# Optimization experiments

Measured on AMD Instinct MI355X. Metric: run time of the kernel, lower is better.

Reference implementation:

```python
import jax, jax.numpy as jnp
import numpy as np

N_NODES = 100000
N_EDGES = 3200000
IN_FEATS = 256
N_UNITS = 32
OUT_FEATS = 40


def setup_inputs() -> dict:
    key = jax.random.key(0)
    k = jax.random.split(key, 6)
    return {
        "x": jax.random.normal(k[0], (N_NODES, IN_FEATS), dtype=jnp.float32),
        "W1": jax.random.normal(k[1], (IN_FEATS, N_UNITS), dtype=jnp.float32) / np.sqrt(IN_FEATS),
        "b1": jnp.zeros((N_UNITS,), dtype=jnp.float32),
        "W2": jax.random.normal(k[2], (N_UNITS, OUT_FEATS), dtype=jnp.float32) / np.sqrt(N_UNITS),
        "b2": jnp.zeros((OUT_FEATS,), dtype=jnp.float32),
        "src": jax.random.randint(k[3], (N_EDGES,), 0, N_NODES, dtype=jnp.int32),
        "dst": jax.random.randint(k[4], (N_EDGES,), 0, N_NODES, dtype=jnp.int32),
    }


def _graph_conv(x, W, b, src, dst, inv_sqrt_out, inv_sqrt_in, n_nodes):
    # DGL GraphConv, norm='both':
    #   out = D_in^{-1/2} * A^T * (D_out^{-1/2} * x @ W) + b
    # Apply the dense transform first (in_feats >= out_feats here) so edge
    # messages are gathered at the narrow width.
    h = (x * inv_sqrt_out[:, None]) @ W              # [N, F_out]
    msgs = h[src]                                     # [E, F_out] gather
    agg = jax.ops.segment_sum(msgs, dst, num_segments=n_nodes)  # [N, F_out]
    return agg * inv_sqrt_in[:, None] + b


def reference(x, W1, b1, W2, b2, src, dst):
    n = x.shape[0]
    ones = jnp.ones((src.shape[0],), dtype=x.dtype)
    out_deg = jax.ops.segment_sum(ones, src, num_segments=n)
    in_deg = jax.ops.segment_sum(ones, dst, num_segments=n)
    inv_sqrt_out = jax.lax.rsqrt(jnp.maximum(out_deg, 1.0))  # DGL clamps deg>=1
    inv_sqrt_in = jax.lax.rsqrt(jnp.maximum(in_deg, 1.0))

    h = _graph_conv(x, W1, b1, src, dst, inv_sqrt_out, inv_sqrt_in, n)
    h = jax.nn.relu(h)
    # dropout(p=0.5, training=False) is identity in eval mode
    h = _graph_conv(h, W2, b2, src, dst, inv_sqrt_out, inv_sqrt_in, n)
    return jax.nn.log_softmax(h, axis=1)
```

## Files before the change

### kernel.cpp

```cpp
#include <hip/hip_runtime.h>
#include <hip/hip_bf16.h>
#include <math.h>

#define N_NODES 100000
#define N_EDGES 3200000
#define IN_FEATS 256
#define N_UNITS 32
#define OUT_FEATS 40

#define NPB 64
#define BSHIFT 6
#define NB 1563
#define CAP 4096

#define NC 49
#define CSHIFT 11
#define CHUNK 8192
#define NBLK ((N_EDGES + CHUNK - 1) / CHUNK)
#define WIN 128

#define ODS2 65536
#define OD_WORDS 16384
#define OD_NSL 2
#define OD_S 192

__global__ void __launch_bounds__(256) outdeg_hist_kernel(const int* __restrict__ src,
                                                          unsigned* __restrict__ partials) {
    __shared__ unsigned lh[OD_WORDS];
    int slice = blockIdx.x / OD_S;
    int stripe = blockIdx.x % OD_S;
    for (int i = threadIdx.x; i < OD_WORDS; i += 256) lh[i] = 0;
    __syncthreads();
    int lo = slice * ODS2;
    const int4* s4 = (const int4*)src;
    const int total4 = N_EDGES / 4;
    for (int i = stripe * 256 + threadIdx.x; i < total4; i += OD_S * 256) {
        int4 v = s4[i];
        unsigned a = (unsigned)(v.x - lo); if (a < ODS2) atomicAdd(&lh[a >> 2], 1u << ((a & 3) * 8));
        unsigned b = (unsigned)(v.y - lo); if (b < ODS2) atomicAdd(&lh[b >> 2], 1u << ((b & 3) * 8));
        unsigned c = (unsigned)(v.z - lo); if (c < ODS2) atomicAdd(&lh[c >> 2], 1u << ((c & 3) * 8));
        unsigned d = (unsigned)(v.w - lo); if (d < ODS2) atomicAdd(&lh[d >> 2], 1u << ((d & 3) * 8));
    }
    __syncthreads();
    unsigned* dstp = partials + (size_t)blockIdx.x * OD_WORDS;
    for (int i = threadIdx.x; i < OD_WORDS; i += 256) dstp[i] = lh[i];
}

__global__ void __launch_bounds__(256) outdeg_reduce_kernel(const unsigned* __restrict__ partials,
                                                            float* __restrict__ inv_out) {
    int i = blockIdx.x * 256 + threadIdx.x;
    if (i >= N_NODES / 4) return;
    int slice = i >> 14;
    int w = i & (OD_WORDS - 1);
    const unsigned* p = partials + (size_t)slice * OD_S * OD_WORDS + w;
    unsigned s = 0;
    #pragma unroll 8
    for (int j = 0; j < OD_S; ++j) s += p[(size_t)j * OD_WORDS];
    float4 r;
    r.x = rsqrtf(fmaxf((float)(s & 0xFF), 1.0f));
    r.y = rsqrtf(fmaxf((float)((s >> 8) & 0xFF), 1.0f));
    r.z = rsqrtf(fmaxf((float)((s >> 16) & 0xFF), 1.0f));
    r.w = rsqrtf(fmaxf((float)(s >> 24), 1.0f));
    *(float4*)(inv_out + 4 * i) = r;
}

__global__ void __launch_bounds__(256) count_kernel(const int* __restrict__ dst,
                                                    int* __restrict__ bucket_count) {
    __shared__ int lh[NB];
    for (int i = threadIdx.x; i < NB; i += 256) lh[i] = 0;
    __syncthreads();
    const int4* d4 = (const int4*)dst;
    const int total4 = N_EDGES / 4;
    for (int i = blockIdx.x * 256 + threadIdx.x; i < total4; i += gridDim.x * 256) {
        int4 v = d4[i];
        atomicAdd(&lh[v.x >> BSHIFT], 1);
        atomicAdd(&lh[v.y >> BSHIFT], 1);
        atomicAdd(&lh[v.z >> BSHIFT], 1);
        atomicAdd(&lh[v.w >> BSHIFT], 1);
    }
    __syncthreads();
    for (int i = threadIdx.x; i < NB; i += 256)
        if (lh[i]) atomicAdd(&bucket_count[i], lh[i]);
}

__global__ void __launch_bounds__(1024) scan_kernel(const int* __restrict__ bucket_count,
                                                    int* __restrict__ gbase,
                                                    int* __restrict__ gcursor,
                                                    int* __restrict__ gbaseA,
                                                    int* __restrict__ gcursorA) {
    __shared__ int ps[1024];
    int t = threadIdx.x;
    int i0 = 2 * t, i1 = 2 * t + 1;
    int a = (i0 < NB) ? bucket_count[i0] : 0;
    int b = (i1 < NB) ? bucket_count[i1] : 0;
    ps[t] = a + b;
    __syncthreads();
    for (int off = 1; off < 1024; off <<= 1) {
        int v = (t >= off) ? ps[t - off] : 0;
        __syncthreads();
        ps[t] += v;
        __syncthreads();
    }
    int excl = ps[t] - (a + b);
    if (i0 < NB) { gbase[i0] = excl; gcursor[i0] = excl; }
    if (i1 <= NB) { gbase[i1] = excl + a; if (i1 < NB) gcursor[i1] = excl + a; }
    __syncthreads();
    if (t < NC) { int v = gbase[t * 32]; gbaseA[t] = v; gcursorA[t] = v; }
    if (t == NC) gbaseA[NC] = N_EDGES;
}

__global__ void __launch_bounds__(512) binA_kernel(const int* __restrict__ src,
                                                   const int* __restrict__ dst,
                                                   int* __restrict__ gcursorA,
                                                   unsigned* __restrict__ pairsA) {
    __shared__ unsigned sortedA[CHUNK];
    __shared__ int hist[NC];
    __shared__ int lstart[NC];
    __shared__ int cur[NC];
    __shared__ int gres[NC];
    int tid = threadIdx.x;
    int e0 = blockIdx.x * CHUNK;
    int cnt = min(CHUNK, N_EDGES - e0);
    unsigned es[16], ed[16];
    #pragma unroll
    for (int r = 0; r < 16; ++r) {
        int idx = tid + 512 * r;
        if (idx < cnt) { es[r] = src[e0 + idx]; ed[r] = dst[e0 + idx]; }
    }
    if (tid < NC) hist[tid] = 0;
    __syncthreads();
    #pragma unroll
    for (int r = 0; r < 16; ++r) {
        int idx = tid + 512 * r;
        if (idx < cnt) atomicAdd(&hist[ed[r] >> CSHIFT], 1);
    }
    __syncthreads();
    if (tid < 64) {
        int v = (tid < NC) ? hist[tid] : 0;
        int inc = v;
        #pragma unroll
        for (int off = 1; off < 64; off <<= 1) {
            int u = __shfl_up(inc, off, 64);
            if ((tid & 63) >= off) inc += u;
        }
        if (tid < NC) {
            int ls = inc - v;
            lstart[tid] = ls;
            cur[tid] = ls;
            gres[tid] = atomicAdd(&gcursorA[tid], v) - ls;
        }
    }
    __syncthreads();
    #pragma unroll
    for (int r = 0; r < 16; ++r) {
        int idx = tid + 512 * r;
        if (idx < cnt) {
            int c = ed[r] >> CSHIFT;
            int pos = atomicAdd(&cur[c], 1);
            sortedA[pos] = es[r] | ((ed[r] & ((1u << CSHIFT) - 1)) << 17);
        }
    }
    __syncthreads();
    for (int i = tid; i < cnt; i += 512) {
        int lo = 0, hi = NC - 1;
        while (lo < hi) { int mid = (lo + hi + 1) >> 1; if (lstart[mid] <= i) lo = mid; else hi = mid - 1; }
        pairsA[gres[lo] + i] = sortedA[i];
    }
}

__global__ void __launch_bounds__(512) binB_kernel(const unsigned* __restrict__ pairsA,
                                                   const int* __restrict__ gbaseA,
                                                   int* __restrict__ gcursor,
                                                   unsigned* __restrict__ pairs) {
    __shared__ unsigned sortedB[CHUNK];
    __shared__ int hist[WIN];
    __shared__ int lstart[WIN];
    __shared__ int cur[WIN];
    __shared__ int gres[WIN];
    __shared__ int gA[NC + 1];
    int tid = threadIdx.x;
    if (tid <= NC) gA[tid] = gbaseA[tid];
    if (tid < WIN) hist[tid] = 0;
    int e0 = blockIdx.x * CHUNK;
    int cnt = min(CHUNK, N_EDGES - e0);
    __syncthreads();
    int c0 = 0;
    { int lo = 0, hi = NC - 1;
      while (lo < hi) { int mid = (lo + hi + 1) >> 1; if (gA[mid] <= e0) lo = mid; else hi = mid - 1; }
      c0 = lo; }
    int w0 = c0 * 32;
    unsigned pv[16]; short fw[16];
    int c = c0;
    #pragma unroll
    for (int r = 0; r < 16; ++r) {
        int idx = tid + 512 * r;
        if (idx < cnt) {
            int pos = e0 + idx;
            while (pos >= gA[c + 1]) ++c;
            unsigned p = pairsA[pos];
            unsigned srcid = p & 0x1FFFF;
            unsigned dl11 = (p >> 17) & 0x7FF;
            int wi = (c - c0) * 32 + (int)(dl11 >> 6);
            atomicAdd(&hist[wi], 1);
            pv[r] = srcid | ((dl11 & 63u) << 24);
            fw[r] = (short)wi;
        }
    }
    __syncthreads();
    if (tid < 64) {
        int v0 = hist[2 * tid], v1 = hist[2 * tid + 1];
        int s = v0 + v1;
        int inc = s;
        #pragma unroll
        for (int off = 1; off < 64; off <<= 1) {
            int u = __shfl_up(inc, off, 64);
            if ((tid & 63) >= off) inc += u;
        }
        int excl = inc - s;
        lstart[2 * tid] = excl;      cur[2 * tid] = excl;
        lstart[2 * tid + 1] = excl + v0; cur[2 * tid + 1] = excl + v0;
        int f0 = w0 + 2 * tid, f1 = f0 + 1;
        gres[2 * tid]     = (f0 < NB) ? (atomicAdd(&gcursor[f0], v0) - excl) : 0;
        gres[2 * tid + 1] = (f1 < NB) ? (atomicAdd(&gcursor[f1], v1) - (excl + v0)) : 0;
    }
    __syncthreads();
    #pragma unroll
    for (int r = 0; r < 16; ++r) {
        int idx = tid + 512 * r;
        if (idx < cnt) {
            int pos = atomicAdd(&cur[fw[r]], 1);
            sortedB[pos] = pv[r];
        }
    }
    __syncthreads();
    for (int i = tid; i < cnt; i += 512) {
        int lo = 0, hi = WIN - 1;
        while (lo < hi) { int mid = (lo + hi + 1) >> 1; if (lstart[mid] <= i) lo = mid; else hi = mid - 1; }
        pairs[gres[lo] + i] = sortedB[i];
    }
}

__global__ void __launch_bounds__(256) gemm1_kernel(
        const float* __restrict__ x, const float* __restrict__ W1,
        const float* __restrict__ inv_out, float* __restrict__ h, int N) {
    __shared__ float Ws[IN_FEATS * N_UNITS];
    for (int idx = threadIdx.x; idx < IN_FEATS * N_UNITS; idx += 256)
        Ws[idx] = W1[idx];
    __syncthreads();
    unsigned t = blockIdx.x * 256 + threadIdx.x;
    unsigned n = t >> 2;
    if (n >= (unsigned)N) return;
    unsigned j0 = (t & 3) * 8;
    float acc[8] = {0, 0, 0, 0, 0, 0, 0, 0};
    const float4* xr = (const float4*)(x + (size_t)n * IN_FEATS);
    #pragma unroll 4
    for (int k4 = 0; k4 < IN_FEATS / 4; ++k4) {
        float4 xv = xr[k4];
        const float* wk = Ws + (k4 * 4) * N_UNITS + j0;
        #pragma unroll
        for (int jj = 0; jj < 8; ++jj) acc[jj] = fmaf(xv.x, wk[jj], acc[jj]);
        #pragma unroll
        for (int jj = 0; jj < 8; ++jj) acc[jj] = fmaf(xv.y, wk[N_UNITS + jj], acc[jj]);
        #pragma unroll
        for (int jj = 0; jj < 8; ++jj) acc[jj] = fmaf(xv.z, wk[2 * N_UNITS + jj], acc[jj]);
        #pragma unroll
        for (int jj = 0; jj < 8; ++jj) acc[jj] = fmaf(xv.w, wk[3 * N_UNITS + jj], acc[jj]);
    }
    float io = inv_out[n];
    float* hr = h + (size_t)n * N_UNITS + j0;
    #pragma unroll
    for (int jj = 0; jj < 8; ++jj) hr[jj] = acc[jj] * io;
}

template <bool LAYER1>
__global__ void __launch_bounds__(256) gather_kernel(
        const float* __restrict__ in, const unsigned* __restrict__ pairs,
        const int* __restrict__ gbase, const float* __restrict__ inv_out,
        const float* __restrict__ b1, float* __restrict__ outbuf,
        float* __restrict__ inv_in) {
    __shared__ int sorted[CAP];
    __shared__ int cnt[NPB];
    __shared__ int start[NPB + 1];
    __shared__ int cur[NPB];
    __shared__ float b1s[N_UNITS];
    int tid = threadIdx.x;
    int b = blockIdx.x;
    int ebeg = gbase[b];
    int ecnt = min(gbase[b + 1] - ebeg, CAP);
    if (tid < NPB) cnt[tid] = 0;
    if (LAYER1 && tid < N_UNITS) b1s[tid] = b1[tid];
    __syncthreads();

    unsigned stash[16];
    #pragma unroll
    for (int r = 0; r < 16; ++r) {
        int idx = tid + 256 * r;
        if (idx < ecnt) {
            unsigned p = pairs[ebeg + idx];
            stash[r] = p;
            atomicAdd(&cnt[p >> 24], 1);
        }
    }
    __syncthreads();

    if (tid < 64) {
        int v = cnt[tid];
        int inc = v;
        #pragma unroll
        for (int off = 1; off < 64; off <<= 1) {
            int u = __shfl_up(inc, off, 64);
            if (tid >= off) inc += u;
        }
        start[tid + 1] = inc;
        cur[tid] = inc - v;
        if (tid == 0) start[0] = 0;
    }
    __syncthreads();

    #pragma unroll
    for (int r = 0; r < 16; ++r) {
        int idx = tid + 256 * r;
        if (idx < ecnt) {
            unsigned p = stash[r];
            int pos = atomicAdd(&cur[p >> 24], 1);
            sorted[pos] = (int)(p & 0xFFFFFF);
        }
    }
    __syncthreads();

    int w = tid >> 6;
    int lane = tid & 63;
    int q = lane & 7;
    int eo = lane >> 3;
    int nd0 = b * NPB;
    #pragma unroll 1
    for (int p = 0; p < 16; ++p) {
        int nd = w * 16 + p;
        int n = nd0 + nd;
        int beg = start[nd];
        int end = start[nd + 1];
        float ax0 = 0.f, ay0 = 0.f, az0 = 0.f, aw0 = 0.f;
        float ax1 = 0.f, ay1 = 0.f, az1 = 0.f, aw1 = 0.f;
        int e = beg + eo;
        for (; e + 8 < end; e += 16) {
            int s0 = sorted[e];
            int s1 = sorted[e + 8];
            float4 v0 = *(const float4*)(in + (size_t)s0 * N_UNITS + q * 4);
            float4 v1 = *(const float4*)(in + (size_t)s1 * N_UNITS + q * 4);
            ax0 += v0.x; ay0 += v0.y; az0 += v0.z; aw0 += v0.w;
            ax1 += v1.x; ay1 += v1.y; az1 += v1.z; aw1 += v1.w;
        }
        if (e < end) {
            float4 v = *(const float4*)(in + (size_t)sorted[e] * N_UNITS + q * 4);
            ax0 += v.x; ay0 += v.y; az0 += v.z; aw0 += v.w;
        }
        e += 8;
        if (e < end) {
            float4 v = *(const float4*)(in + (size_t)sorted[e] * N_UNITS + q * 4);
            ax1 += v.x; ay1 += v.y; az1 += v.z; aw1 += v.w;
        }
        float sx = ax0 + ax1, sy = ay0 + ay1, sz = az0 + az1, sw = aw0 + aw1;
        #pragma unroll
        for (int st = 8; st < 64; st <<= 1) {
            sx += __shfl_xor(sx, st, 64);
            sy += __shfl_xor(sy, st, 64);
            sz += __shfl_xor(sz, st, 64);
            sw += __shfl_xor(sw, st, 64);
        }
        if (eo == 0 && n < N_NODES) {
            if (LAYER1) {
                float ii = rsqrtf(fmaxf((float)(end - beg), 1.0f));
                float io = inv_out[n];
                float4 r;
                r.x = fmaxf(fmaf(sx, ii, b1s[q * 4 + 0]), 0.0f) * io;
                r.y = fmaxf(fmaf(sy, ii, b1s[q * 4 + 1]), 0.0f) * io;
                r.z = fmaxf(fmaf(sz, ii, b1s[q * 4 + 2]), 0.0f) * io;
                r.w = fmaxf(fmaf(sw, ii, b1s[q * 4 + 3]), 0.0f) * io;
                *(float4*)(outbuf + (size_t)n * N_UNITS + q * 4) = r;
                if (q == 0) inv_in[n] = ii;
            } else {
                *(float4*)(outbuf + (size_t)n * N_UNITS + q * 4) =
                    make_float4(sx, sy, sz, sw);
            }
        }
    }
}

__global__ void __launch_bounds__(256) finalize_kernel(
        const float* __restrict__ agg2, const float* __restrict__ inv_in,
        const float* __restrict__ W2, const float* __restrict__ b2,
        float* __restrict__ out, int N) {
    __shared__ float W2s[N_UNITS * OUT_FEATS];
    __shared__ float b2s[OUT_FEATS];
    for (int i = threadIdx.x; i < N_UNITS * OUT_FEATS; i += 256) W2s[i] = W2[i];
    if (threadIdx.x < OUT_FEATS) b2s[threadIdx.x] = b2[threadIdx.x];
    __syncthreads();
    int n = blockIdx.x * 256 + threadIdx.x;
    if (n >= N) return;
    float a[N_UNITS];
    const float4* ar = (const float4*)(agg2 + (size_t)n * N_UNITS);
    #pragma unroll
    for (int qq = 0; qq < N_UNITS / 4; ++qq) {
        float4 v = ar[qq];
        a[qq * 4 + 0] = v.x; a[qq * 4 + 1] = v.y; a[qq * 4 + 2] = v.z; a[qq * 4 + 3] = v.w;
    }
    float ii = inv_in[n];
    float s[OUT_FEATS];
    #pragma unroll
    for (int o = 0; o < OUT_FEATS; ++o) s[o] = 0.0f;
    #pragma unroll
    for (int k = 0; k < N_UNITS; ++k) {
        float ak = a[k];
        #pragma unroll
        for (int o = 0; o < OUT_FEATS; ++o) s[o] = fmaf(ak, W2s[k * OUT_FEATS + o], s[o]);
    }
    float mx = -INFINITY;
    #pragma unroll
    for (int o = 0; o < OUT_FEATS; ++o) {
        s[o] = fmaf(s[o], ii, b2s[o]);
        mx = fmaxf(mx, s[o]);
    }
    float sum = 0.0f;
    #pragma unroll
    for (int o = 0; o < OUT_FEATS; ++o) sum += __expf(s[o] - mx);
    float lse = mx + __logf(sum);
    #pragma unroll
    for (int o = 0; o < OUT_FEATS; ++o) s[o] -= lse;
    float4* orow4 = (float4*)(out + (size_t)n * OUT_FEATS);
    #pragma unroll
    for (int qq = 0; qq < OUT_FEATS / 4; ++qq)
        orow4[qq] = make_float4(s[qq * 4], s[qq * 4 + 1], s[qq * 4 + 2], s[qq * 4 + 3]);
}

extern "C" void kernel_launch(void* const* d_in, const int* in_sizes, int n_in,
                              void* d_out, int out_size, void* d_ws, size_t ws_size,
                              hipStream_t stream) {
    const float* x   = (const float*)d_in[0];
    const float* W1  = (const float*)d_in[1];
    const float* b1  = (const float*)d_in[2];
    const float* W2  = (const float*)d_in[3];
    const float* b2  = (const float*)d_in[4];
    const int*   src = (const int*)d_in[5];
    const int*   dst = (const int*)d_in[6];
    float* out = (float*)d_out;

    char* base = (char*)d_ws;
    float*    inv_out      = (float*)(base);
    int*      bucket_count = (int*)(base + 400000L);
    int*      gbaseA       = (int*)(base + 406400L);
    int*      gcursorA     = (int*)(base + 406912L);
    int*      gbase        = (int*)(base + 408192L);
    int*      gcursor      = (int*)(base + 416384L);
    float*    inv_in       = (float*)(base + 424576L);
    unsigned* pairs        = (unsigned*)(base + 824576L);
    float*    h            = (float*)(base + 13624576L);
    float*    rprime       = (float*)(base + 26424576L);
    float*    agg2         = (float*)(base + 39224576L);
    unsigned* pairsA       = (unsigned*)h;
    unsigned* partials     = (unsigned*)rprime;

    hipMemsetAsync(bucket_count, 0, 8192L, stream);

    outdeg_hist_kernel<<<OD_NSL * OD_S, 256, 0, stream>>>(src, partials);
    outdeg_reduce_kernel<<<(N_NODES / 4 + 255) / 256, 256, 0, stream>>>(partials, inv_out);

    count_kernel<<<128, 256, 0, stream>>>(dst, bucket_count);
    scan_kernel<<<1, 1024, 0, stream>>>(bucket_count, gbase, gcursor, gbaseA, gcursorA);
    binA_kernel<<<NBLK, 512, 0, stream>>>(src, dst, gcursorA, pairsA);
    binB_kernel<<<NBLK, 512, 0, stream>>>(pairsA, gbaseA, gcursor, pairs);

    gemm1_kernel<<<(N_NODES * 4 + 255) / 256, 256, 0, stream>>>(x, W1, inv_out, h, N_NODES);

    gather_kernel<true><<<NB, 256, 0, stream>>>(h, pairs, gbase, inv_out, b1, rprime, inv_in);
    gather_kernel<false><<<NB, 256, 0, stream>>>(rprime, pairs, gbase, inv_out, b1, agg2, inv_in);

    finalize_kernel<<<(N_NODES + 255) / 256, 256, 0, stream>>>(agg2, inv_in, W2, b2, out, N_NODES);
}
```

Baseline: 387.7 us.

## Compute full output row per thread in gemm1, read W1 via uniform loads

Rewrites the first dense transform so each thread computes all 32 outputs of one node rather than 8, dropping the shared-memory staging of W1 and reading weights directly from global memory with wave-uniform addresses (likely scalar/broadcast loads). This cuts redundant re-reads of each x row by four threads and the shared-memory fill and barrier, and stores the result as float4. In exchange it needs many more registers per thread (32 accumulators), and x rows are now read with a large per-thread stride, which hurts coalescing.

```diff
diff --git a/kernel.cpp b/kernel.cpp
--- a/kernel.cpp
+++ b/kernel.cpp
@@ -240,36 +240,40 @@
     }
 }
 
-__global__ void __launch_bounds__(256) gemm1_kernel(
+#define G1_TPB 128
+__global__ void __launch_bounds__(G1_TPB) gemm1_kernel(
         const float* __restrict__ x, const float* __restrict__ W1,
         const float* __restrict__ inv_out, float* __restrict__ h, int N) {
-    __shared__ float Ws[IN_FEATS * N_UNITS];
-    for (int idx = threadIdx.x; idx < IN_FEATS * N_UNITS; idx += 256)
-        Ws[idx] = W1[idx];
-    __syncthreads();
-    unsigned t = blockIdx.x * 256 + threadIdx.x;
-    unsigned n = t >> 2;
-    if (n >= (unsigned)N) return;
-    unsigned j0 = (t & 3) * 8;
-    float acc[8] = {0, 0, 0, 0, 0, 0, 0, 0};
+    int n = blockIdx.x * G1_TPB + threadIdx.x;
+    if (n >= N) return;
+    float acc[N_UNITS];
+    #pragma unroll
+    for (int j = 0; j < N_UNITS; ++j) acc[j] = 0.f;
     const float4* xr = (const float4*)(x + (size_t)n * IN_FEATS);
-    #pragma unroll 4
+    #pragma unroll 2
     for (int k4 = 0; k4 < IN_FEATS / 4; ++k4) {
         float4 xv = xr[k4];
-        const float* wk = Ws + (k4 * 4) * N_UNITS + j0;
-        #pragma unroll
-        for (int jj = 0; jj < 8; ++jj) acc[jj] = fmaf(xv.x, wk[jj], acc[jj]);
-        #pragma unroll
-        for (int jj = 0; jj < 8; ++jj) acc[jj] = fmaf(xv.y, wk[N_UNITS + jj], acc[jj]);
-        #pragma unroll
-        for (int jj = 0; jj < 8; ++jj) acc[jj] = fmaf(xv.z, wk[2 * N_UNITS + jj], acc[jj]);
-        #pragma unroll
-        for (int jj = 0; jj < 8; ++jj) acc[jj] = fmaf(xv.w, wk[3 * N_UNITS + jj], acc[jj]);
+        const float* wk = W1 + (k4 * 4) * N_UNITS;
+        #pragma unroll
+        for (int j = 0; j < N_UNITS; ++j) acc[j] = fmaf(xv.x, wk[j], acc[j]);
+        #pragma unroll
+        for (int j = 0; j < N_UNITS; ++j) acc[j] = fmaf(xv.y, wk[N_UNITS + j], acc[j]);
+        #pragma unroll
+        for (int j = 0; j < N_UNITS; ++j) acc[j] = fmaf(xv.z, wk[2 * N_UNITS + j], acc[j]);
+        #pragma unroll
+        for (int j = 0; j < N_UNITS; ++j) acc[j] = fmaf(xv.w, wk[3 * N_UNITS + j], acc[j]);
     }
     float io = inv_out[n];
-    float* hr = h + (size_t)n * N_UNITS + j0;
-    #pragma unroll
-    for (int jj = 0; jj < 8; ++jj) hr[jj] = acc[jj] * io;
+    float4* hr = (float4*)(h + (size_t)n * N_UNITS);
+    #pragma unroll
+    for (int q = 0; q < N_UNITS / 4; ++q) {
+        float4 r;
+        r.x = acc[q * 4 + 0] * io;
+        r.y = acc[q * 4 + 1] * io;
+        r.z = acc[q * 4 + 2] * io;
+        r.w = acc[q * 4 + 3] * io;
+        hr[q] = r;
+    }
 }
 
 template <bool LAYER1>
@@ -469,7 +473,7 @@
     binA_kernel<<<NBLK, 512, 0, stream>>>(src, dst, gcursorA, pairsA);
     binB_kernel<<<NBLK, 512, 0, stream>>>(pairsA, gbaseA, gcursor, pairs);
 
-    gemm1_kernel<<<(N_NODES * 4 + 255) / 256, 256, 0, stream>>>(x, W1, inv_out, h, N_NODES);
+    gemm1_kernel<<<(N_NODES + G1_TPB - 1) / G1_TPB, G1_TPB, 0, stream>>>(x, W1, inv_out, h, N_NODES);
 
     gather_kernel<true><<<NB, 256, 0, stream>>>(h, pairs, gbase, inv_out, b1, rprime, inv_in);
     gather_kernel<false><<<NB, 256, 0, stream>>>(rprime, pairs, gbase, inv_out, b1, agg2, inv_in);
```

After: 435.4 us. +12.3%, slower.

## Fuse layer-2 dense transform and log-softmax into the second gather kernel

Applied to the files above, without the earlier changes.

The separate finalize kernel is removed. The second-layer gather now keeps each block's aggregated rows in shared memory, then applies W2, the bias, in-degree normalisation and log-softmax directly, with four threads per node each producing ten outputs and combining max and sum through shuffles. This avoids writing and re-reading the agg2 intermediate and saves one launch, at the cost of extra shared memory and register pressure in the gather. The gemm1 kernel also moves to 512-thread blocks with float4 weight staging.

```diff
diff --git a/kernel.cpp b/kernel.cpp
--- a/kernel.cpp
+++ b/kernel.cpp
@@ -240,14 +240,15 @@
     }
 }
 
-__global__ void __launch_bounds__(256) gemm1_kernel(
+#define G1_TPB 512
+__global__ void __launch_bounds__(G1_TPB, 8) gemm1_kernel(
         const float* __restrict__ x, const float* __restrict__ W1,
         const float* __restrict__ inv_out, float* __restrict__ h, int N) {
     __shared__ float Ws[IN_FEATS * N_UNITS];
-    for (int idx = threadIdx.x; idx < IN_FEATS * N_UNITS; idx += 256)
-        Ws[idx] = W1[idx];
-    __syncthreads();
-    unsigned t = blockIdx.x * 256 + threadIdx.x;
+    for (int idx = threadIdx.x; idx < IN_FEATS * N_UNITS / 4; idx += G1_TPB)
+        ((float4*)Ws)[idx] = ((const float4*)W1)[idx];
+    __syncthreads();
+    unsigned t = blockIdx.x * G1_TPB + threadIdx.x;
     unsigned n = t >> 2;
     if (n >= (unsigned)N) return;
     unsigned j0 = (t & 3) * 8;
@@ -277,18 +278,27 @@
         const float* __restrict__ in, const unsigned* __restrict__ pairs,
         const int* __restrict__ gbase, const float* __restrict__ inv_out,
         const float* __restrict__ b1, float* __restrict__ outbuf,
-        float* __restrict__ inv_in) {
+        float* __restrict__ inv_in,
+        const float* __restrict__ W2, const float* __restrict__ b2,
+        float* __restrict__ final_out) {
     __shared__ int sorted[CAP];
     __shared__ int cnt[NPB];
     __shared__ int start[NPB + 1];
     __shared__ int cur[NPB];
-    __shared__ float b1s[N_UNITS];
+    __shared__ float b1s[LAYER1 ? N_UNITS : 1];
+    __shared__ float agg_s[LAYER1 ? 1 : NPB][LAYER1 ? 1 : 36];
+    __shared__ float W2s[LAYER1 ? 1 : N_UNITS * OUT_FEATS];
+    __shared__ float b2s[LAYER1 ? 1 : OUT_FEATS];
     int tid = threadIdx.x;
     int b = blockIdx.x;
     int ebeg = gbase[b];
     int ecnt = min(gbase[b + 1] - ebeg, CAP);
     if (tid < NPB) cnt[tid] = 0;
     if (LAYER1 && tid < N_UNITS) b1s[tid] = b1[tid];
+    if (!LAYER1) {
+        for (int i = tid; i < N_UNITS * OUT_FEATS; i += 256) W2s[i] = W2[i];
+        if (tid < OUT_FEATS) b2s[tid] = b2[tid];
+    }
     __syncthreads();
 
     unsigned stash[16];
@@ -367,69 +377,72 @@
             sz += __shfl_xor(sz, st, 64);
             sw += __shfl_xor(sw, st, 64);
         }
-        if (eo == 0 && n < N_NODES) {
+        if (eo == 0) {
             if (LAYER1) {
-                float ii = rsqrtf(fmaxf((float)(end - beg), 1.0f));
-                float io = inv_out[n];
-                float4 r;
-                r.x = fmaxf(fmaf(sx, ii, b1s[q * 4 + 0]), 0.0f) * io;
-                r.y = fmaxf(fmaf(sy, ii, b1s[q * 4 + 1]), 0.0f) * io;
-                r.z = fmaxf(fmaf(sz, ii, b1s[q * 4 + 2]), 0.0f) * io;
-                r.w = fmaxf(fmaf(sw, ii, b1s[q * 4 + 3]), 0.0f) * io;
-                *(float4*)(outbuf + (size_t)n * N_UNITS + q * 4) = r;
-                if (q == 0) inv_in[n] = ii;
+                if (n < N_NODES) {
+                    float ii = rsqrtf(fmaxf((float)(end - beg), 1.0f));
+                    float io = inv_out[n];
+                    float4 r;
+                    r.x = fmaxf(fmaf(sx, ii, b1s[q * 4 + 0]), 0.0f) * io;
+                    r.y = fmaxf(fmaf(sy, ii, b1s[q * 4 + 1]), 0.0f) * io;
+                    r.z = fmaxf(fmaf(sz, ii, b1s[q * 4 + 2]), 0.0f) * io;
+                    r.w = fmaxf(fmaf(sw, ii, b1s[q * 4 + 3]), 0.0f) * io;
+                    *(float4*)(outbuf + (size_t)n * N_UNITS + q * 4) = r;
+                    if (q == 0) inv_in[n] = ii;
+                }
             } else {
-                *(float4*)(outbuf + (size_t)n * N_UNITS + q * 4) =
-                    make_float4(sx, sy, sz, sw);
+                agg_s[nd][q * 4 + 0] = sx;
+                agg_s[nd][q * 4 + 1] = sy;
+                agg_s[nd][q * 4 + 2] = sz;
+                agg_s[nd][q * 4 + 3] = sw;
             }
         }
     }
-}
-
-__global__ void __launch_bounds__(256) finalize_kernel(
-        const float* __restrict__ agg2, const float* __restrict__ inv_in,
-        const float* __restrict__ W2, const float* __restrict__ b2,
-        float* __restrict__ out, int N) {
-    __shared__ float W2s[N_UNITS * OUT_FEATS];
-    __shared__ float b2s[OUT_FEATS];
-    for (int i = threadIdx.x; i < N_UNITS * OUT_FEATS; i += 256) W2s[i] = W2[i];
-    if (threadIdx.x < OUT_FEATS) b2s[threadIdx.x] = b2[threadIdx.x];
-    __syncthreads();
-    int n = blockIdx.x * 256 + threadIdx.x;
-    if (n >= N) return;
-    float a[N_UNITS];
-    const float4* ar = (const float4*)(agg2 + (size_t)n * N_UNITS);
-    #pragma unroll
-    for (int qq = 0; qq < N_UNITS / 4; ++qq) {
-        float4 v = ar[qq];
-        a[qq * 4 + 0] = v.x; a[qq * 4 + 1] = v.y; a[qq * 4 + 2] = v.z; a[qq * 4 + 3] = v.w;
-    }
-    float ii = inv_in[n];
-    float s[OUT_FEATS];
-    #pragma unroll
-    for (int o = 0; o < OUT_FEATS; ++o) s[o] = 0.0f;
-    #pragma unroll
-    for (int k = 0; k < N_UNITS; ++k) {
-        float ak = a[k];
-        #pragma unroll
-        for (int o = 0; o < OUT_FEATS; ++o) s[o] = fmaf(ak, W2s[k * OUT_FEATS + o], s[o]);
-    }
-    float mx = -INFINITY;
-    #pragma unroll
-    for (int o = 0; o < OUT_FEATS; ++o) {
-        s[o] = fmaf(s[o], ii, b2s[o]);
-        mx = fmaxf(mx, s[o]);
-    }
-    float sum = 0.0f;
-    #pragma unroll
-    for (int o = 0; o < OUT_FEATS; ++o) sum += __expf(s[o] - mx);
-    float lse = mx + __logf(sum);
-    #pragma unroll
-    for (int o = 0; o < OUT_FEATS; ++o) s[o] -= lse;
-    float4* orow4 = (float4*)(out + (size_t)n * OUT_FEATS);
-    #pragma unroll
-    for (int qq = 0; qq < OUT_FEATS / 4; ++qq)
-        orow4[qq] = make_float4(s[qq * 4], s[qq * 4 + 1], s[qq * 4 + 2], s[qq * 4 + 3]);
+
+    if (!LAYER1) {
+        __syncthreads();
+        int nd = tid >> 2;
+        int part = tid & 3;
+        int n = nd0 + nd;
+        float a[N_UNITS];
+        #pragma unroll
+        for (int qq = 0; qq < 8; ++qq) {
+            float4 v = *(const float4*)&agg_s[nd][qq * 4];
+            a[qq * 4 + 0] = v.x; a[qq * 4 + 1] = v.y;
+            a[qq * 4 + 2] = v.z; a[qq * 4 + 3] = v.w;
+        }
+        float ii = rsqrtf(fmaxf((float)(start[nd + 1] - start[nd]), 1.0f));
+        float s[10];
+        #pragma unroll
+        for (int o = 0; o < 10; ++o) s[o] = 0.0f;
+        const float* w2p = W2s + part * 10;
+        #pragma unroll
+        for (int k = 0; k < N_UNITS; ++k) {
+            float ak = a[k];
+            #pragma unroll
+            for (int o = 0; o < 10; ++o) s[o] = fmaf(ak, w2p[k * OUT_FEATS + o], s[o]);
+        }
+        float mx = -INFINITY;
+        #pragma unroll
+        for (int o = 0; o < 10; ++o) {
+            s[o] = fmaf(s[o], ii, b2s[part * 10 + o]);
+            mx = fmaxf(mx, s[o]);
+        }
+        mx = fmaxf(mx, __shfl_xor(mx, 1, 64));
+        mx = fmaxf(mx, __shfl_xor(mx, 2, 64));
+        float sum = 0.0f;
+        #pragma unroll
+        for (int o = 0; o < 10; ++o) sum += __expf(s[o] - mx);
+        sum += __shfl_xor(sum, 1, 64);
+        sum += __shfl_xor(sum, 2, 64);
+        float lse = mx + __logf(sum);
+        if (n < N_NODES) {
+            float2* op = (float2*)(final_out + (size_t)n * OUT_FEATS + part * 10);
+            #pragma unroll
+            for (int u = 0; u < 5; ++u)
+                op[u] = make_float2(s[2 * u] - lse, s[2 * u + 1] - lse);
+        }
+    }
 }
 
 extern "C" void kernel_launch(void* const* d_in, const int* in_sizes, int n_in,
@@ -469,10 +482,10 @@
     binA_kernel<<<NBLK, 512, 0, stream>>>(src, dst, gcursorA, pairsA);
     binB_kernel<<<NBLK, 512, 0, stream>>>(pairsA, gbaseA, gcursor, pairs);
 
-    gemm1_kernel<<<(N_NODES * 4 + 255) / 256, 256, 0, stream>>>(x, W1, inv_out, h, N_NODES);
-
-    gather_kernel<true><<<NB, 256, 0, stream>>>(h, pairs, gbase, inv_out, b1, rprime, inv_in);
-    gather_kernel<false><<<NB, 256, 0, stream>>>(rprime, pairs, gbase, inv_out, b1, agg2, inv_in);
-
-    finalize_kernel<<<(N_NODES + 255) / 256, 256, 0, stream>>>(agg2, inv_in, W2, b2, out, N_NODES);
-}
+    gemm1_kernel<<<(N_NODES * 4 + G1_TPB - 1) / G1_TPB, G1_TPB, 0, stream>>>(x, W1, inv_out, h, N_NODES);
+
+    gather_kernel<true><<<NB, 256, 0, stream>>>(h, pairs, gbase, inv_out, b1, rprime, inv_in,
+                                                W2, b2, out);
+    gather_kernel<false><<<NB, 256, 0, stream>>>(rprime, pairs, gbase, inv_out, b1, agg2, inv_in,
+                                                 W2, b2, out);
+}
```

Result: slower. 413.7 us (+6.7%).

## Merge independent preprocessing kernels into combined launches via block-index dispatch

Applied to the files above, without the earlier changes.

Merges the out-degree histogram and dst bucket count into one launch, the prefix scan and the out-degree reduction into another, and the first-layer binning pass and the dense GEMM into a third. Blocks branch on their block index, so work that does not depend on the other half runs concurrently and launch overhead and tail gaps shrink. The buffers are rearranged so h no longer aliases pairsA: h now shares agg2's slot, which is written only after h is consumed. The cost is larger shared-memory allocations for the smaller branches, which may lower occupancy, and the GEMM now uses 512-thread blocks.

```diff
diff --git a/kernel.cpp b/kernel.cpp
--- a/kernel.cpp
+++ b/kernel.cpp
@@ -23,148 +23,191 @@
 #define OD_WORDS 16384
 #define OD_NSL 2
 #define OD_S 192
-
-__global__ void __launch_bounds__(256) outdeg_hist_kernel(const int* __restrict__ src,
-                                                          unsigned* __restrict__ partials) {
-    __shared__ unsigned lh[OD_WORDS];
-    int slice = blockIdx.x / OD_S;
-    int stripe = blockIdx.x % OD_S;
-    for (int i = threadIdx.x; i < OD_WORDS; i += 256) lh[i] = 0;
-    __syncthreads();
-    int lo = slice * ODS2;
-    const int4* s4 = (const int4*)src;
-    const int total4 = N_EDGES / 4;
-    for (int i = stripe * 256 + threadIdx.x; i < total4; i += OD_S * 256) {
-        int4 v = s4[i];
-        unsigned a = (unsigned)(v.x - lo); if (a < ODS2) atomicAdd(&lh[a >> 2], 1u << ((a & 3) * 8));
-        unsigned b = (unsigned)(v.y - lo); if (b < ODS2) atomicAdd(&lh[b >> 2], 1u << ((b & 3) * 8));
-        unsigned c = (unsigned)(v.z - lo); if (c < ODS2) atomicAdd(&lh[c >> 2], 1u << ((c & 3) * 8));
-        unsigned d = (unsigned)(v.w - lo); if (d < ODS2) atomicAdd(&lh[d >> 2], 1u << ((d & 3) * 8));
-    }
-    __syncthreads();
-    unsigned* dstp = partials + (size_t)blockIdx.x * OD_WORDS;
-    for (int i = threadIdx.x; i < OD_WORDS; i += 256) dstp[i] = lh[i];
-}
-
-__global__ void __launch_bounds__(256) outdeg_reduce_kernel(const unsigned* __restrict__ partials,
-                                                            float* __restrict__ inv_out) {
-    int i = blockIdx.x * 256 + threadIdx.x;
-    if (i >= N_NODES / 4) return;
-    int slice = i >> 14;
-    int w = i & (OD_WORDS - 1);
-    const unsigned* p = partials + (size_t)slice * OD_S * OD_WORDS + w;
-    unsigned s = 0;
-    #pragma unroll 8
-    for (int j = 0; j < OD_S; ++j) s += p[(size_t)j * OD_WORDS];
-    float4 r;
-    r.x = rsqrtf(fmaxf((float)(s & 0xFF), 1.0f));
-    r.y = rsqrtf(fmaxf((float)((s >> 8) & 0xFF), 1.0f));
-    r.z = rsqrtf(fmaxf((float)((s >> 16) & 0xFF), 1.0f));
-    r.w = rsqrtf(fmaxf((float)(s >> 24), 1.0f));
-    *(float4*)(inv_out + 4 * i) = r;
-}
-
-__global__ void __launch_bounds__(256) count_kernel(const int* __restrict__ dst,
-                                                    int* __restrict__ bucket_count) {
-    __shared__ int lh[NB];
-    for (int i = threadIdx.x; i < NB; i += 256) lh[i] = 0;
-    __syncthreads();
-    const int4* d4 = (const int4*)dst;
-    const int total4 = N_EDGES / 4;
-    for (int i = blockIdx.x * 256 + threadIdx.x; i < total4; i += gridDim.x * 256) {
-        int4 v = d4[i];
-        atomicAdd(&lh[v.x >> BSHIFT], 1);
-        atomicAdd(&lh[v.y >> BSHIFT], 1);
-        atomicAdd(&lh[v.z >> BSHIFT], 1);
-        atomicAdd(&lh[v.w >> BSHIFT], 1);
-    }
-    __syncthreads();
-    for (int i = threadIdx.x; i < NB; i += 256)
-        if (lh[i]) atomicAdd(&bucket_count[i], lh[i]);
-}
-
-__global__ void __launch_bounds__(1024) scan_kernel(const int* __restrict__ bucket_count,
-                                                    int* __restrict__ gbase,
-                                                    int* __restrict__ gcursor,
-                                                    int* __restrict__ gbaseA,
-                                                    int* __restrict__ gcursorA) {
+#define HIST_NBLK (OD_NSL * OD_S)
+#define COUNT_NBLK 128
+
+#define GEMM_NBLK ((N_NODES + 127) / 128)
+
+__global__ void __launch_bounds__(256) histcount_kernel(const int* __restrict__ src,
+                                                        const int* __restrict__ dst,
+                                                        unsigned* __restrict__ partials,
+                                                        int* __restrict__ bucket_count) {
+    __shared__ __align__(16) char smem[OD_WORDS * 4];
+    int tid = threadIdx.x;
+    if (blockIdx.x < HIST_NBLK) {
+        unsigned* lh = (unsigned*)smem;
+        int slice = blockIdx.x / OD_S;
+        int stripe = blockIdx.x % OD_S;
+        for (int i = tid; i < OD_WORDS; i += 256) lh[i] = 0;
+        __syncthreads();
+        int lo = slice * ODS2;
+        const int4* s4 = (const int4*)src;
+        const int total4 = N_EDGES / 4;
+        for (int i = stripe * 256 + tid; i < total4; i += OD_S * 256) {
+            int4 v = s4[i];
+            unsigned a = (unsigned)(v.x - lo); if (a < ODS2) atomicAdd(&lh[a >> 2], 1u << ((a & 3) * 8));
+            unsigned b = (unsigned)(v.y - lo); if (b < ODS2) atomicAdd(&lh[b >> 2], 1u << ((b & 3) * 8));
+            unsigned c = (unsigned)(v.z - lo); if (c < ODS2) atomicAdd(&lh[c >> 2], 1u << ((c & 3) * 8));
+            unsigned d = (unsigned)(v.w - lo); if (d < ODS2) atomicAdd(&lh[d >> 2], 1u << ((d & 3) * 8));
+        }
+        __syncthreads();
+        unsigned* dstp = partials + (size_t)blockIdx.x * OD_WORDS;
+        for (int i = tid; i < OD_WORDS; i += 256) dstp[i] = lh[i];
+    } else {
+        int* lh = (int*)smem;
+        int cb = blockIdx.x - HIST_NBLK;
+        for (int i = tid; i < NB; i += 256) lh[i] = 0;
+        __syncthreads();
+        const int4* d4 = (const int4*)dst;
+        const int total4 = N_EDGES / 4;
+        for (int i = cb * 256 + tid; i < total4; i += COUNT_NBLK * 256) {
+            int4 v = d4[i];
+            atomicAdd(&lh[v.x >> BSHIFT], 1);
+            atomicAdd(&lh[v.y >> BSHIFT], 1);
+            atomicAdd(&lh[v.z >> BSHIFT], 1);
+            atomicAdd(&lh[v.w >> BSHIFT], 1);
+        }
+        __syncthreads();
+        for (int i = tid; i < NB; i += 256)
+            if (lh[i]) atomicAdd(&bucket_count[i], lh[i]);
+    }
+}
+
+__global__ void __launch_bounds__(1024) scanreduce_kernel(const int* __restrict__ bucket_count,
+                                                          int* __restrict__ gbase,
+                                                          int* __restrict__ gcursor,
+                                                          int* __restrict__ gbaseA,
+                                                          int* __restrict__ gcursorA,
+                                                          const unsigned* __restrict__ partials,
+                                                          float* __restrict__ inv_out) {
     __shared__ int ps[1024];
     int t = threadIdx.x;
-    int i0 = 2 * t, i1 = 2 * t + 1;
-    int a = (i0 < NB) ? bucket_count[i0] : 0;
-    int b = (i1 < NB) ? bucket_count[i1] : 0;
-    ps[t] = a + b;
-    __syncthreads();
-    for (int off = 1; off < 1024; off <<= 1) {
-        int v = (t >= off) ? ps[t - off] : 0;
-        __syncthreads();
-        ps[t] += v;
-        __syncthreads();
-    }
-    int excl = ps[t] - (a + b);
-    if (i0 < NB) { gbase[i0] = excl; gcursor[i0] = excl; }
-    if (i1 <= NB) { gbase[i1] = excl + a; if (i1 < NB) gcursor[i1] = excl + a; }
-    __syncthreads();
-    if (t < NC) { int v = gbase[t * 32]; gbaseA[t] = v; gcursorA[t] = v; }
-    if (t == NC) gbaseA[NC] = N_EDGES;
-}
-
-__global__ void __launch_bounds__(512) binA_kernel(const int* __restrict__ src,
-                                                   const int* __restrict__ dst,
-                                                   int* __restrict__ gcursorA,
-                                                   unsigned* __restrict__ pairsA) {
-    __shared__ unsigned sortedA[CHUNK];
-    __shared__ int hist[NC];
-    __shared__ int lstart[NC];
-    __shared__ int cur[NC];
-    __shared__ int gres[NC];
+    if (blockIdx.x == 0) {
+        int i0 = 2 * t, i1 = 2 * t + 1;
+        int a = (i0 < NB) ? bucket_count[i0] : 0;
+        int b = (i1 < NB) ? bucket_count[i1] : 0;
+        ps[t] = a + b;
+        __syncthreads();
+        for (int off = 1; off < 1024; off <<= 1) {
+            int v = (t >= off) ? ps[t - off] : 0;
+            __syncthreads();
+            ps[t] += v;
+            __syncthreads();
+        }
+        int excl = ps[t] - (a + b);
+        if (i0 < NB) { gbase[i0] = excl; gcursor[i0] = excl; }
+        if (i1 <= NB) { gbase[i1] = excl + a; if (i1 < NB) gcursor[i1] = excl + a; }
+        __syncthreads();
+        if (t < NC) { int v = gbase[t * 32]; gbaseA[t] = v; gcursorA[t] = v; }
+        if (t == NC) gbaseA[NC] = N_EDGES;
+    } else {
+        int i = (blockIdx.x - 1) * 1024 + t;
+        if (i >= N_NODES / 4) return;
+        int slice = i >> 14;
+        int w = i & (OD_WORDS - 1);
+        const unsigned* p = partials + (size_t)slice * OD_S * OD_WORDS + w;
+        unsigned s = 0;
+        #pragma unroll 8
+        for (int j = 0; j < OD_S; ++j) s += p[(size_t)j * OD_WORDS];
+        float4 r;
+        r.x = rsqrtf(fmaxf((float)(s & 0xFF), 1.0f));
+        r.y = rsqrtf(fmaxf((float)((s >> 8) & 0xFF), 1.0f));
+        r.z = rsqrtf(fmaxf((float)((s >> 16) & 0xFF), 1.0f));
+        r.w = rsqrtf(fmaxf((float)(s >> 24), 1.0f));
+        *(float4*)(inv_out + 4 * i) = r;
+    }
+}
+
+__global__ void __launch_bounds__(512) binA_gemm_kernel(const int* __restrict__ src,
+                                                        const int* __restrict__ dst,
+                                                        int* __restrict__ gcursorA,
+                                                        unsigned* __restrict__ pairsA,
+                                                        const float* __restrict__ x,
+                                                        const float* __restrict__ W1,
+                                                        const float* __restrict__ inv_out,
+                                                        float* __restrict__ h, int N) {
+    __shared__ __align__(16) char smem[CHUNK * 4 + 4 * NC * 4];
     int tid = threadIdx.x;
-    int e0 = blockIdx.x * CHUNK;
-    int cnt = min(CHUNK, N_EDGES - e0);
-    unsigned es[16], ed[16];
-    #pragma unroll
-    for (int r = 0; r < 16; ++r) {
-        int idx = tid + 512 * r;
-        if (idx < cnt) { es[r] = src[e0 + idx]; ed[r] = dst[e0 + idx]; }
-    }
-    if (tid < NC) hist[tid] = 0;
-    __syncthreads();
-    #pragma unroll
-    for (int r = 0; r < 16; ++r) {
-        int idx = tid + 512 * r;
-        if (idx < cnt) atomicAdd(&hist[ed[r] >> CSHIFT], 1);
-    }
-    __syncthreads();
-    if (tid < 64) {
-        int v = (tid < NC) ? hist[tid] : 0;
-        int inc = v;
-        #pragma unroll
-        for (int off = 1; off < 64; off <<= 1) {
-            int u = __shfl_up(inc, off, 64);
-            if ((tid & 63) >= off) inc += u;
-        }
-        if (tid < NC) {
-            int ls = inc - v;
-            lstart[tid] = ls;
-            cur[tid] = ls;
-            gres[tid] = atomicAdd(&gcursorA[tid], v) - ls;
-        }
-    }
-    __syncthreads();
-    #pragma unroll
-    for (int r = 0; r < 16; ++r) {
-        int idx = tid + 512 * r;
-        if (idx < cnt) {
-            int c = ed[r] >> CSHIFT;
-            int pos = atomicAdd(&cur[c], 1);
-            sortedA[pos] = es[r] | ((ed[r] & ((1u << CSHIFT) - 1)) << 17);
-        }
-    }
-    __syncthreads();
-    for (int i = tid; i < cnt; i += 512) {
-        int lo = 0, hi = NC - 1;
-        while (lo < hi) { int mid = (lo + hi + 1) >> 1; if (lstart[mid] <= i) lo = mid; else hi = mid - 1; }
-        pairsA[gres[lo] + i] = sortedA[i];
+    if (blockIdx.x < NBLK) {
+        unsigned* sortedA = (unsigned*)smem;
+        int* hist   = (int*)(smem + CHUNK * 4);
+        int* lstart = hist + NC;
+        int* cur    = lstart + NC;
+        int* gres   = cur + NC;
+        int e0 = blockIdx.x * CHUNK;
+        int cnt = min(CHUNK, N_EDGES - e0);
+        unsigned es[16], ed[16];
+        #pragma unroll
+        for (int r = 0; r < 16; ++r) {
+            int idx = tid + 512 * r;
+            if (idx < cnt) { es[r] = src[e0 + idx]; ed[r] = dst[e0 + idx]; }
+        }
+        if (tid < NC) hist[tid] = 0;
+        __syncthreads();
+        #pragma unroll
+        for (int r = 0; r < 16; ++r) {
+            int idx = tid + 512 * r;
+            if (idx < cnt) atomicAdd(&hist[ed[r] >> CSHIFT], 1);
+        }
+        __syncthreads();
+        if (tid < 64) {
+            int v = (tid < NC) ? hist[tid] : 0;
+            int inc = v;
+            #pragma unroll
+            for (int off = 1; off < 64; off <<= 1) {
+                int u = __shfl_up(inc, off, 64);
+                if ((tid & 63) >= off) inc += u;
+            }
+            if (tid < NC) {
+                int ls = inc - v;
+                lstart[tid] = ls;
+                cur[tid] = ls;
+                gres[tid] = atomicAdd(&gcursorA[tid], v) - ls;
+            }
+        }
+        __syncthreads();
+        #pragma unroll
+        for (int r = 0; r < 16; ++r) {
+            int idx = tid + 512 * r;
+            if (idx < cnt) {
+                int c = ed[r] >> CSHIFT;
+                int pos = atomicAdd(&cur[c], 1);
+                sortedA[pos] = es[r] | ((ed[r] & ((1u << CSHIFT) - 1)) << 17);
+            }
+        }
+        __syncthreads();
+        for (int i = tid; i < cnt; i += 512) {
+            int lo = 0, hi = NC - 1;
+            while (lo < hi) { int mid = (lo + hi + 1) >> 1; if (lstart[mid] <= i) lo = mid; else hi = mid - 1; }
+            pairsA[gres[lo] + i] = sortedA[i];
+        }
+    } else {
+        float* Ws = (float*)smem;
+        for (int idx = tid; idx < IN_FEATS * N_UNITS / 4; idx += 512)
+            ((float4*)Ws)[idx] = ((const float4*)W1)[idx];
+        __syncthreads();
+        unsigned n = (unsigned)(blockIdx.x - NBLK) * 128 + (tid >> 2);
+        if (n >= (unsigned)N) return;
+        unsigned j0 = (tid & 3) * 8;
+        float acc[8] = {0, 0, 0, 0, 0, 0, 0, 0};
+        const float4* xr = (const float4*)(x + (size_t)n * IN_FEATS);
+        #pragma unroll 4
+        for (int k4 = 0; k4 < IN_FEATS / 4; ++k4) {
+            float4 xv = xr[k4];
+            const float* wk = Ws + (k4 * 4) * N_UNITS + j0;
+            #pragma unroll
+            for (int jj = 0; jj < 8; ++jj) acc[jj] = fmaf(xv.x, wk[jj], acc[jj]);
+            #pragma unroll
+            for (int jj = 0; jj < 8; ++jj) acc[jj] = fmaf(xv.y, wk[N_UNITS + jj], acc[jj]);
+            #pragma unroll
+            for (int jj = 0; jj < 8; ++jj) acc[jj] = fmaf(xv.z, wk[2 * N_UNITS + jj], acc[jj]);
+            #pragma unroll
+            for (int jj = 0; jj < 8; ++jj) acc[jj] = fmaf(xv.w, wk[3 * N_UNITS + jj], acc[jj]);
+        }
+        float io = inv_out[n];
+        float* hr = h + (size_t)n * N_UNITS + j0;
+        #pragma unroll
+        for (int jj = 0; jj < 8; ++jj) hr[jj] = acc[jj] * io;
     }
 }
 
@@ -238,38 +281,6 @@
         while (lo < hi) { int mid = (lo + hi + 1) >> 1; if (lstart[mid] <= i) lo = mid; else hi = mid - 1; }
         pairs[gres[lo] + i] = sortedB[i];
     }
-}
-
-__global__ void __launch_bounds__(256) gemm1_kernel(
-        const float* __restrict__ x, const float* __restrict__ W1,
-        const float* __restrict__ inv_out, float* __restrict__ h, int N) {
-    __shared__ float Ws[IN_FEATS * N_UNITS];
-    for (int idx = threadIdx.x; idx < IN_FEATS * N_UNITS; idx += 256)
-        Ws[idx] = W1[idx];
-    __syncthreads();
-    unsigned t = blockIdx.x * 256 + threadIdx.x;
-    unsigned n = t >> 2;
-    if (n >= (unsigned)N) return;
-    unsigned j0 = (t & 3) * 8;
-    float acc[8] = {0, 0, 0, 0, 0, 0, 0, 0};
-    const float4* xr = (const float4*)(x + (size_t)n * IN_FEATS);
-    #pragma unroll 4
-    for (int k4 = 0; k4 < IN_FEATS / 4; ++k4) {
-        float4 xv = xr[k4];
-        const float* wk = Ws + (k4 * 4) * N_UNITS + j0;
-        #pragma unroll
-        for (int jj = 0; jj < 8; ++jj) acc[jj] = fmaf(xv.x, wk[jj], acc[jj]);
-        #pragma unroll
-        for (int jj = 0; jj < 8; ++jj) acc[jj] = fmaf(xv.y, wk[N_UNITS + jj], acc[jj]);
-        #pragma unroll
-        for (int jj = 0; jj < 8; ++jj) acc[jj] = fmaf(xv.z, wk[2 * N_UNITS + jj], acc[jj]);
-        #pragma unroll
-        for (int jj = 0; jj < 8; ++jj) acc[jj] = fmaf(xv.w, wk[3 * N_UNITS + jj], acc[jj]);
-    }
-    float io = inv_out[n];
-    float* hr = h + (size_t)n * N_UNITS + j0;
-    #pragma unroll
-    for (int jj = 0; jj < 8; ++jj) hr[jj] = acc[jj] * io;
 }
 
 template <bool LAYER1>
@@ -453,23 +464,22 @@
     int*      gcursor      = (int*)(base + 416384L);
     float*    inv_in       = (float*)(base + 424576L);
     unsigned* pairs        = (unsigned*)(base + 824576L);
-    float*    h            = (float*)(base + 13624576L);
+    unsigned* pairsA       = (unsigned*)(base + 13624576L);
     float*    rprime       = (float*)(base + 26424576L);
+    float*    h            = (float*)(base + 39224576L);
     float*    agg2         = (float*)(base + 39224576L);
-    unsigned* pairsA       = (unsigned*)h;
     unsigned* partials     = (unsigned*)rprime;
 
     hipMemsetAsync(bucket_count, 0, 8192L, stream);
 
-    outdeg_hist_kernel<<<OD_NSL * OD_S, 256, 0, stream>>>(src, partials);
-    outdeg_reduce_kernel<<<(N_NODES / 4 + 255) / 256, 256, 0, stream>>>(partials, inv_out);
-
-    count_kernel<<<128, 256, 0, stream>>>(dst, bucket_count);
-    scan_kernel<<<1, 1024, 0, stream>>>(bucket_count, gbase, gcursor, gbaseA, gcursorA);
-    binA_kernel<<<NBLK, 512, 0, stream>>>(src, dst, gcursorA, pairsA);
+    histcount_kernel<<<HIST_NBLK + COUNT_NBLK, 256, 0, stream>>>(src, dst, partials, bucket_count);
+    scanreduce_kernel<<<1 + (N_NODES / 4 + 1023) / 1024, 1024, 0, stream>>>(
+        bucket_count, gbase, gcursor, gbaseA, gcursorA, partials, inv_out);
+
+    binA_gemm_kernel<<<NBLK + GEMM_NBLK, 512, 0, stream>>>(
+        src, dst, gcursorA, pairsA, x, W1, inv_out, h, N_NODES);
+
     binB_kernel<<<NBLK, 512, 0, stream>>>(pairsA, gbaseA, gcursor, pairs);
-
-    gemm1_kernel<<<(N_NODES * 4 + 255) / 256, 256, 0, stream>>>(x, W1, inv_out, h, N_NODES);
 
     gather_kernel<true><<<NB, 256, 0, stream>>>(h, pairs, gbase, inv_out, b1, rprime, inv_in);
     gather_kernel<false><<<NB, 256, 0, stream>>>(rprime, pairs, gbase, inv_out, b1, agg2, inv_in);
```

New measurement: 363.6 us. -6.2%, faster.
